# Performance work log

Hardware: AMD Instinct MI355X
Metric: run time of the kernel (lower is better)

## Reference

```python
import jax, jax.numpy as jnp
import numpy as np

W1 = 7          # half window
W2 = 2 * W1 + 1 # window size = 15
H = 4           # num heads
DH = 64         # head dim
DO = H * DH     # 256


def setup_inputs() -> dict:
    key = jax.random.key(0)
    ks = jax.random.split(key, 7)
    B, T, D = 2, 4096, 768
    s = 1.0 / np.sqrt(D).astype(np.float32)
    inputs = jax.random.normal(ks[0], (B, T, D), dtype=jnp.float32)
    Wq = jax.random.normal(ks[1], (DO, D), dtype=jnp.float32) * s
    bq = jax.random.normal(ks[2], (DO,), dtype=jnp.float32) * s
    Wv = jax.random.normal(ks[3], (DO, D), dtype=jnp.float32) * s
    bv = jax.random.normal(ks[4], (DO,), dtype=jnp.float32) * s
    pos_emb = jax.random.normal(ks[5], (W2, D), dtype=jnp.float32)
    return {"inputs": inputs, "Wq": Wq, "bq": bq, "Wv": Wv, "bv": bv, "pos_emb": pos_emb}


def reference(inputs, Wq, bq, Wv, bv, pos_emb):
    # Faithful to the torch module: k uses the *query* projection (source bug),
    # no softmax, no 1/sqrt(d) scaling.
    B, T, D = inputs.shape
    pad = jnp.pad(inputs, ((0, 0), (W1, W1), (0, 0)))  # [B, T+2*W1, D]
    # Project once on the padded sequence, then gather windows (linear ops
    # commute with the window gather; position bias added post-projection).
    q_pad = pad @ Wq.T + bq            # [B, T+2*W1, DO]
    v_pad = pad @ Wv.T + bv            # [B, T+2*W1, DO]
    pos_q = pos_emb @ Wq.T             # [W2, DO]  (query(window+pos) = query(window)+pos@Wq^T)
    pos_v = pos_emb @ Wv.T             # [W2, DO]
    idx = jnp.arange(T)[:, None] + jnp.arange(W2)[None, :]  # [T, W2]
    k = q_pad[:, idx] + pos_q          # [B, T, W2, DO]
    v = v_pad[:, idx] + pos_v          # [B, T, W2, DO]
    q = inputs @ Wq.T + bq             # [B, T, DO]
    qh = q.reshape(B, T, H, DH)
    kh = k.reshape(B, T, W2, H, DH)
    vh = v.reshape(B, T, W2, H, DH)
    scores = jnp.einsum('bthd,btwhd->bthw', qh, kh)   # [B, T, H, W2] (no softmax)
    ctx = jnp.einsum('bthw,btwhd->bthd', scores, vh)  # [B, T, H, DH]
    return ctx.reshape(B, T, DO)
```

## Files before the change

### kernel.cpp

```cpp
#include <hip/hip_runtime.h>

#define TPC   4110
#define MROWS 8220
#define MTOT  8235
#define MPAD  8320
#define KD    768

typedef __attribute__((ext_vector_type(8))) short short8;
typedef __attribute__((ext_vector_type(4))) float f32x4;

#define LOAD_LDS16(gp, lp)                                                   \
  __builtin_amdgcn_global_load_lds(                                          \
      (const __attribute__((address_space(1))) void*)(gp),                   \
      (__attribute__((address_space(3))) void*)(lp), 16, 0, 0)

__device__ inline unsigned bfr(float x) {
  unsigned u = __float_as_uint(x);
  return (u + 0x7FFFu + ((u >> 16) & 1u)) >> 16;
}
__device__ inline unsigned pack2(float a, float b) {
  return bfr(a) | (bfr(b) << 16);
}
__device__ inline float bflo(unsigned u) { return __uint_as_float(u << 16); }
__device__ inline float bfhi(unsigned u) { return __uint_as_float(u & 0xffff0000u); }

__global__ __launch_bounds__(256) void cast_w(
    const float* __restrict__ Wq, const float* __restrict__ Wv,
    ushort* __restrict__ Wbf) {
  int gid = blockIdx.x * 256 + threadIdx.x;
  int row = gid / 96, c = (gid - row * 96) * 8;
  const float* src = (row < 256) ? Wq + (size_t)row * KD + c
                                 : Wv + (size_t)(row - 256) * KD + c;
  float4 f0 = *(const float4*)src;
  float4 f1 = *(const float4*)(src + 4);
  uint4 o;
  o.x = pack2(f0.x, f0.y); o.y = pack2(f0.z, f0.w);
  o.z = pack2(f1.x, f1.y); o.w = pack2(f1.z, f1.w);
  *(uint4*)(Wbf + (size_t)row * KD + c) = o;
}

__global__ __launch_bounds__(256) void gemm_bf16(
    const float* __restrict__ inp, const float* __restrict__ pos,
    const ushort* __restrict__ Wbf,
    const float* __restrict__ bq, const float* __restrict__ bv,
    ushort* __restrict__ q_out, ushort* __restrict__ v_out,
    ushort* __restrict__ pos_q, ushort* __restrict__ pos_v) {
  __shared__ ushort Al[2][64 * 64];
  __shared__ ushort Bl[2][128 * 64];
  const int tid = threadIdx.x;
  const int wave = tid >> 6, lane = tid & 63;
  const int lin = blockIdx.x;
  const int wg = (lin & 7) * 65 + (lin >> 3);
  const int ns = wg & 3;
  const int m0 = (wg >> 2) * 64;
  const int wm = wave & 1, wn = wave >> 1;
  const int fr = lane & 15, quad = lane >> 4;

  const float* agf[2];
  int aoff[2];
  #pragma unroll
  for (int i = 0; i < 2; i++) {
    int c = i * 256 + tid, row = c >> 3, kq = c & 7;
    int m = m0 + row;
    aoff[i] = c * 8;
    const float* s = nullptr;
    if (m < MROWS) {
      int bb = (m >= TPC) ? 1 : 0;
      int t = m - bb * TPC - 7;
      if (t >= 0 && t < 4096)
        s = inp + ((size_t)bb * 4096 + t) * KD + ((kq ^ (row & 7)) * 8);
    } else if (m < MTOT) {
      s = pos + (size_t)(m - MROWS) * KD + ((kq ^ (row & 7)) * 8);
    }
    agf[i] = s;
  }
  const ushort* bg[4];
  #pragma unroll
  for (int i = 0; i < 4; i++) {
    int c = i * 256 + tid, row = c >> 3, kq = c & 7;
    bg[i] = Wbf + (size_t)(ns * 128 + row) * KD + ((kq ^ (row & 7)) * 8);
  }

  f32x4 acc[2][4];
  #pragma unroll
  for (int i = 0; i < 2; i++)
    #pragma unroll
    for (int j = 0; j < 4; j++) acc[i][j] = 0.0f;

  float4 fa[2][2];

#define STAGE_A_LOAD(k0)                                                     \
  do {                                                                       \
    _Pragma("unroll")                                                        \
    for (int i = 0; i < 2; i++) {                                            \
      if (agf[i]) {                                                          \
        fa[i][0] = *(const float4*)(agf[i] + (k0));                          \
        fa[i][1] = *(const float4*)(agf[i] + (k0) + 4);                      \
      } else {                                                               \
        fa[i][0] = make_float4(0.f, 0.f, 0.f, 0.f);                         \
        fa[i][1] = make_float4(0.f, 0.f, 0.f, 0.f);                         \
      }                                                                      \
    }                                                                        \
  } while (0)

#define STAGE_A_WRITE(bsel)                                                  \
  do {                                                                       \
    _Pragma("unroll")                                                        \
    for (int i = 0; i < 2; i++) {                                            \
      uint4 o;                                                               \
      o.x = pack2(fa[i][0].x, fa[i][0].y);                                   \
      o.y = pack2(fa[i][0].z, fa[i][0].w);                                   \
      o.z = pack2(fa[i][1].x, fa[i][1].y);                                   \
      o.w = pack2(fa[i][1].z, fa[i][1].w);                                   \
      *(uint4*)(&Al[bsel][0] + aoff[i]) = o;                                 \
    }                                                                        \
  } while (0)

#define STAGE_B(bsel, k0)                                                    \
  do {                                                                       \
    _Pragma("unroll")                                                        \
    for (int i = 0; i < 4; i++)                                              \
      LOAD_LDS16(bg[i] + (k0), &Bl[bsel][0] + (i * 256 + wave * 64) * 8);    \
  } while (0)

#define COMPUTE(bsel)                                                        \
  do {                                                                       \
    short8 afr[2][2], bfrag[2][4];                                           \
    _Pragma("unroll")                                                        \
    for (int ks = 0; ks < 2; ks++) {                                         \
      const int e = ((ks * 4 + quad) ^ (fr & 7)) * 8;        \
      _Pragma("unroll")                                                      \
      for (int i = 0; i < 2; i++)                                            \
        afr[ks][i] =                                                         \
            *(const short8*)(&Al[bsel][0] + (wm * 32 + i * 16 + fr) * 64 + e);\
      _Pragma("unroll")                                                      \
      for (int j = 0; j < 4; j++)                                            \
        bfrag[ks][j] =                                                       \
            *(const short8*)(&Bl[bsel][0] + (wn * 64 + j * 16 + fr) * 64 + e);\
    }                                                                        \
    _Pragma("unroll")                                                        \
    for (int ks = 0; ks < 2; ks++)                                           \
      _Pragma("unroll")                                                      \
      for (int i = 0; i < 2; i++)                                            \
        _Pragma("unroll")                                                    \
        for (int j = 0; j < 4; j++)                                          \
          acc[i][j] = __builtin_amdgcn_mfma_f32_16x16x32_bf16(               \
              afr[ks][i], bfrag[ks][j], acc[i][j], 0, 0, 0);                 \
  } while (0)

  STAGE_A_LOAD(0);
  STAGE_B(0, 0);
  STAGE_A_WRITE(0);
  __syncthreads();
  #pragma unroll 1
  for (int k0 = 0; k0 < 640; k0 += 128) {
    STAGE_A_LOAD(k0 + 64);
    STAGE_B(1, k0 + 64);
    COMPUTE(0);
    STAGE_A_WRITE(1);
    __syncthreads();
    STAGE_A_LOAD(k0 + 128);
    STAGE_B(0, k0 + 128);
    COMPUTE(1);
    STAGE_A_WRITE(0);
    __syncthreads();
  }
  STAGE_A_LOAD(704);
  STAGE_B(1, 704);
  COMPUTE(0);
  STAGE_A_WRITE(1);
  __syncthreads();
  COMPUTE(1);

#undef STAGE_A_LOAD
#undef STAGE_A_WRITE
#undef STAGE_B
#undef COMPUTE

  const float* bias = (ns < 2) ? bq : bv;
  ushort* outp = (ns < 2) ? q_out : v_out;
  ushort* posp = (ns < 2) ? pos_q : pos_v;
  const int wbase = (ns & 1) * 128;
  #pragma unroll
  for (int j = 0; j < 4; j++) {
    const int colq = wbase + wn * 64 + j * 16 + fr;
    const int h = colq >> 6, d = colq & 63;
    const float bj = bias[colq];
    #pragma unroll
    for (int i = 0; i < 2; i++) {
      const int mb = m0 + wm * 32 + i * 16 + quad * 4;
      #pragma unroll
      for (int r = 0; r < 4; r++) {
        const int m = mb + r;
        if (m < MROWS) {
          int b = m / TPC, tp = m - b * TPC;
          outp[(((size_t)(b * 4 + h)) * TPC + tp) * 64 + d] =
              (ushort)bfr(acc[i][j][r] + bj);
        } else if (m < MTOT) {
          posp[(m - MROWS) * 256 + colq] = (ushort)bfr(acc[i][j][r]);
        }
      }
    }
  }
}

__global__ __launch_bounds__(256) void win_attn4(
    const ushort* __restrict__ q_out, const ushort* __restrict__ v_out,
    const ushort* __restrict__ pos_q, const ushort* __restrict__ pos_v,
    float* __restrict__ out) {
  __shared__ __align__(16) float ks[78][68];
  __shared__ __align__(16) float vs[78][68];
  __shared__ __align__(16) float pq[15][68];
  __shared__ __align__(16) float pv[15][68];
  const int tid = threadIdx.x;
  const int bh = blockIdx.x >> 6, tile = blockIdx.x & 63;
  const int b = bh >> 2, h = bh & 3;
  const int t0 = tile * 64;

  const size_t slab = (((size_t)(b * 4 + h)) * TPC + t0) * 64;
  for (int idx = tid; idx < 624; idx += 256) {
    int row = idx >> 3, c8 = (idx & 7) * 8;
    uint4 kc = *(const uint4*)(q_out + slab + idx * 8);
    ks[row][c8 + 0] = bflo(kc.x); ks[row][c8 + 1] = bfhi(kc.x);
    ks[row][c8 + 2] = bflo(kc.y); ks[row][c8 + 3] = bfhi(kc.y);
    ks[row][c8 + 4] = bflo(kc.z); ks[row][c8 + 5] = bfhi(kc.z);
    ks[row][c8 + 6] = bflo(kc.w); ks[row][c8 + 7] = bfhi(kc.w);
    uint4 vc = *(const uint4*)(v_out + slab + idx * 8);
    vs[row][c8 + 0] = bflo(vc.x); vs[row][c8 + 1] = bfhi(vc.x);
    vs[row][c8 + 2] = bflo(vc.y); vs[row][c8 + 3] = bfhi(vc.y);
    vs[row][c8 + 4] = bflo(vc.z); vs[row][c8 + 5] = bfhi(vc.z);
    vs[row][c8 + 6] = bflo(vc.w); vs[row][c8 + 7] = bfhi(vc.w);
  }
  if (tid < 120) {
    int row = tid >> 3, c8 = (tid & 7) * 8;
    uint4 qc = *(const uint4*)(pos_q + row * 256 + h * 64 + c8);
    pq[row][c8 + 0] = bflo(qc.x); pq[row][c8 + 1] = bfhi(qc.x);
    pq[row][c8 + 2] = bflo(qc.y); pq[row][c8 + 3] = bfhi(qc.y);
    pq[row][c8 + 4] = bflo(qc.z); pq[row][c8 + 5] = bfhi(qc.z);
    pq[row][c8 + 6] = bflo(qc.w); pq[row][c8 + 7] = bfhi(qc.w);
    uint4 vc = *(const uint4*)(pos_v + row * 256 + h * 64 + c8);
    pv[row][c8 + 0] = bflo(vc.x); pv[row][c8 + 1] = bfhi(vc.x);
    pv[row][c8 + 2] = bflo(vc.y); pv[row][c8 + 3] = bfhi(vc.y);
    pv[row][c8 + 4] = bflo(vc.z); pv[row][c8 + 5] = bfhi(vc.z);
    pv[row][c8 + 6] = bflo(vc.w); pv[row][c8 + 7] = bfhi(vc.w);
  }
  __syncthreads();

  const int tl = tid >> 2, qtr = tid & 3, d0 = qtr * 16;
  float4 qv[4];
  #pragma unroll
  for (int c = 0; c < 4; c++) qv[c] = *(float4*)&ks[tl + 7][d0 + c * 4];
  float4 ctx[4];
  #pragma unroll
  for (int c = 0; c < 4; c++) ctx[c] = make_float4(0.f, 0.f, 0.f, 0.f);

  #pragma unroll
  for (int w = 0; w < 15; w++) {
    float p = 0.f;
    #pragma unroll
    for (int c = 0; c < 4; c++) {
      float4 kk = *(float4*)&ks[tl + w][d0 + c * 4];
      float4 pp = *(float4*)&pq[w][d0 + c * 4];
      p += qv[c].x * (kk.x + pp.x) + qv[c].y * (kk.y + pp.y) +
           qv[c].z * (kk.z + pp.z) + qv[c].w * (kk.w + pp.w);
    }
    p += __shfl_xor(p, 1, 64);
    p += __shfl_xor(p, 2, 64);
    #pragma unroll
    for (int c = 0; c < 4; c++) {
      float4 vv = *(float4*)&vs[tl + w][d0 + c * 4];
      float4 pp = *(float4*)&pv[w][d0 + c * 4];
      ctx[c].x += p * (vv.x + pp.x);
      ctx[c].y += p * (vv.y + pp.y);
      ctx[c].z += p * (vv.z + pp.z);
      ctx[c].w += p * (vv.w + pp.w);
    }
  }
  size_t oo = ((size_t)(b * 4096 + t0 + tl)) * 256 + h * 64 + d0;
  #pragma unroll
  for (int c = 0; c < 4; c++) *(float4*)(out + oo + c * 4) = ctx[c];
}

extern "C" void kernel_launch(void* const* d_in, const int* in_sizes, int n_in,
                              void* d_out, int out_size, void* d_ws,
                              size_t ws_size, hipStream_t stream) {
  const float* inp = (const float*)d_in[0];
  const float* Wq  = (const float*)d_in[1];
  const float* bq  = (const float*)d_in[2];
  const float* Wv  = (const float*)d_in[3];
  const float* bv  = (const float*)d_in[4];
  const float* pos = (const float*)d_in[5];
  float* out = (float*)d_out;

  char* ws = (char*)d_ws;
  ushort* Wbf   = (ushort*)ws;
  ushort* q_out = (ushort*)(ws + 786432);
  ushort* v_out = (ushort*)(ws + 4995072);
  ushort* pos_q = (ushort*)(ws + 9203712);
  ushort* pos_v = (ushort*)(ws + 9211392);

  hipLaunchKernelGGL(cast_w, dim3(192), dim3(256), 0, stream, Wq, Wv, Wbf);
  hipLaunchKernelGGL(gemm_bf16, dim3(520), dim3(256), 0, stream,
                     inp, pos, Wbf, bq, bv, q_out, v_out, pos_q, pos_v);
  hipLaunchKernelGGL(win_attn4, dim3(2 * 4 * 64), dim3(256), 0, stream,
                     q_out, v_out, pos_q, pos_v, out);
}
```

Baseline: 107.9 us.

## Load A fragments directly from global into registers, bypassing LDS

The A operand tile is no longer staged through shared memory. Each lane now loads the fp32 elements it needs for its MFMA fragments straight from global memory, converts them to bf16 in registers, and feeds them to the MFMAs. This removes the LDS writes and reads for A and halves shared memory use. In exchange, A rows are re-read by both waves that share a row block (wn=0,1), global accesses become less coalesced (32-byte chunks per lane with stride), and register pressure rises because double-buffered fp32 data is now held in registers.

```diff
diff --git a/kernel.cpp b/kernel.cpp
--- a/kernel.cpp
+++ b/kernel.cpp
@@ -45,7 +45,6 @@
     const float* __restrict__ bq, const float* __restrict__ bv,
     ushort* __restrict__ q_out, ushort* __restrict__ v_out,
     ushort* __restrict__ pos_q, ushort* __restrict__ pos_v) {
-  __shared__ ushort Al[2][64 * 64];
   __shared__ ushort Bl[2][128 * 64];
   const int tid = threadIdx.x;
   const int wave = tid >> 6, lane = tid & 63;
@@ -57,20 +56,17 @@
   const int fr = lane & 15, quad = lane >> 4;
 
   const float* agf[2];
-  int aoff[2];
   #pragma unroll
   for (int i = 0; i < 2; i++) {
-    int c = i * 256 + tid, row = c >> 3, kq = c & 7;
-    int m = m0 + row;
-    aoff[i] = c * 8;
+    int m = m0 + wm * 32 + i * 16 + fr;
     const float* s = nullptr;
     if (m < MROWS) {
       int bb = (m >= TPC) ? 1 : 0;
       int t = m - bb * TPC - 7;
       if (t >= 0 && t < 4096)
-        s = inp + ((size_t)bb * 4096 + t) * KD + ((kq ^ (row & 7)) * 8);
+        s = inp + ((size_t)bb * 4096 + t) * KD + quad * 8;
     } else if (m < MTOT) {
-      s = pos + (size_t)(m - MROWS) * KD + ((kq ^ (row & 7)) * 8);
+      s = pos + (size_t)(m - MROWS) * KD + quad * 8;
     }
     agf[i] = s;
   }
@@ -87,33 +83,42 @@
     #pragma unroll
     for (int j = 0; j < 4; j++) acc[i][j] = 0.0f;
 
-  float4 fa[2][2];
-
-#define STAGE_A_LOAD(k0)                                                     \
+  float4 fa[2][2][2];
+  short8 afr[2][2];
+
+#define A_LOAD(k0)                                                           \
   do {                                                                       \
     _Pragma("unroll")                                                        \
     for (int i = 0; i < 2; i++) {                                            \
       if (agf[i]) {                                                          \
-        fa[i][0] = *(const float4*)(agf[i] + (k0));                          \
-        fa[i][1] = *(const float4*)(agf[i] + (k0) + 4);                      \
+        _Pragma("unroll")                                                    \
+        for (int ks = 0; ks < 2; ks++) {                                     \
+          fa[i][ks][0] = *(const float4*)(agf[i] + (k0) + ks * 32);          \
+          fa[i][ks][1] = *(const float4*)(agf[i] + (k0) + ks * 32 + 4);      \
+        }                                                                    \
       } else {                                                               \
-        fa[i][0] = make_float4(0.f, 0.f, 0.f, 0.f);                         \
-        fa[i][1] = make_float4(0.f, 0.f, 0.f, 0.f);                         \
+        _Pragma("unroll")                                                    \
+        for (int ks = 0; ks < 2; ks++) {                                     \
+          fa[i][ks][0] = make_float4(0.f, 0.f, 0.f, 0.f);                    \
+          fa[i][ks][1] = make_float4(0.f, 0.f, 0.f, 0.f);                    \
+        }                                                                    \
       }                                                                      \
     }                                                                        \
   } while (0)
 
-#define STAGE_A_WRITE(bsel)                                                  \
+#define A_CVT()                                                              \
   do {                                                                       \
     _Pragma("unroll")                                                        \
-    for (int i = 0; i < 2; i++) {                                            \
-      uint4 o;                                                               \
-      o.x = pack2(fa[i][0].x, fa[i][0].y);                                   \
-      o.y = pack2(fa[i][0].z, fa[i][0].w);                                   \
-      o.z = pack2(fa[i][1].x, fa[i][1].y);                                   \
-      o.w = pack2(fa[i][1].z, fa[i][1].w);                                   \
-      *(uint4*)(&Al[bsel][0] + aoff[i]) = o;                                 \
-    }                                                                        \
+    for (int i = 0; i < 2; i++)                                              \
+      _Pragma("unroll")                                                      \
+      for (int ks = 0; ks < 2; ks++) {                                       \
+        uint4 o;                                                             \
+        o.x = pack2(fa[i][ks][0].x, fa[i][ks][0].y);                         \
+        o.y = pack2(fa[i][ks][0].z, fa[i][ks][0].w);                         \
+        o.z = pack2(fa[i][ks][1].x, fa[i][ks][1].y);                         \
+        o.w = pack2(fa[i][ks][1].z, fa[i][ks][1].w);                         \
+        afr[ks][i] = *(short8*)&o;                                           \
+      }                                                                      \
   } while (0)
 
 #define STAGE_B(bsel, k0)                                                    \
@@ -125,14 +130,10 @@
 
 #define COMPUTE(bsel)                                                        \
   do {                                                                       \
-    short8 afr[2][2], bfrag[2][4];                                           \
+    short8 bfrag[2][4];                                                      \
     _Pragma("unroll")                                                        \
     for (int ks = 0; ks < 2; ks++) {                                         \
       const int e = ((ks * 4 + quad) ^ (fr & 7)) * 8;        \
-      _Pragma("unroll")                                                      \
-      for (int i = 0; i < 2; i++)                                            \
-        afr[ks][i] =                                                         \
-            *(const short8*)(&Al[bsel][0] + (wm * 32 + i * 16 + fr) * 64 + e);\
       _Pragma("unroll")                                                      \
       for (int j = 0; j < 4; j++)                                            \
         bfrag[ks][j] =                                                       \
@@ -148,32 +149,32 @@
               afr[ks][i], bfrag[ks][j], acc[i][j], 0, 0, 0);                 \
   } while (0)
 
-  STAGE_A_LOAD(0);
+  A_LOAD(0);
   STAGE_B(0, 0);
-  STAGE_A_WRITE(0);
+  A_CVT();
   __syncthreads();
   #pragma unroll 1
   for (int k0 = 0; k0 < 640; k0 += 128) {
-    STAGE_A_LOAD(k0 + 64);
+    A_LOAD(k0 + 64);
     STAGE_B(1, k0 + 64);
     COMPUTE(0);
-    STAGE_A_WRITE(1);
+    A_CVT();
     __syncthreads();
-    STAGE_A_LOAD(k0 + 128);
+    A_LOAD(k0 + 128);
     STAGE_B(0, k0 + 128);
     COMPUTE(1);
-    STAGE_A_WRITE(0);
+    A_CVT();
     __syncthreads();
   }
-  STAGE_A_LOAD(704);
+  A_LOAD(704);
   STAGE_B(1, 704);
   COMPUTE(0);
-  STAGE_A_WRITE(1);
+  A_CVT();
   __syncthreads();
   COMPUTE(1);
 
-#undef STAGE_A_LOAD
-#undef STAGE_A_WRITE
+#undef A_LOAD
+#undef A_CVT
 #undef STAGE_B
 #undef COMPUTE
 
```

Result: slower. 133.4 us (+23.6%).
